# Optimization experiments

Hardware: AMD Instinct MI355X
Metric: run time of the kernel (lower is better)

The kernel has to match this reference:

```python
import jax, jax.numpy as jnp
import numpy as np

B, N, O, K, F = 4, 256, 5, 5, 256
H, D, DFF = 4, 64, 1024  # num_heads, KQ_len, FFN hidden
EPS = 1e-5


def setup_inputs() -> dict:
    key = jax.random.key(0)
    ks = jax.random.split(key, 16)
    s = 0.05
    p = lambda k, shape: (jax.random.normal(k, shape, jnp.float32) * s)
    return {
        "x": jax.random.normal(ks[0], (B, N, O, K, K, F), jnp.float32),
        "Wq": p(ks[1], (H * D, F)), "bq": p(ks[2], (H * D,)),
        "Wk": p(ks[3], (H * D, F)), "bk": p(ks[4], (H * D,)),
        "Wv": p(ks[5], (H * D, F)), "bv": p(ks[6], (H * D,)),
        "Wf": p(ks[7], (F, F)), "bf": p(ks[8], (F,)),
        "ln1_w": jnp.ones((N, O, F), jnp.float32), "ln1_b": jnp.zeros((N, O, F), jnp.float32),
        "ln2_w": jnp.ones((N, O, F), jnp.float32), "ln2_b": jnp.zeros((N, O, F), jnp.float32),
        "W1": p(ks[9], (DFF, F)), "b1": p(ks[10], (DFF,)),
        "W2": p(ks[11], (F, DFF)), "b2": p(ks[12], (F,)),
    }


def _layer_norm3(x, w, b):
    # torch LayerNorm with normalized_shape=[N, O, F]: stats over last 3 dims
    mu = jnp.mean(x, axis=(1, 2, 3), keepdims=True)
    var = jnp.var(x, axis=(1, 2, 3), keepdims=True)
    return (x - mu) * jax.lax.rsqrt(var + EPS) * w + b


def _split_heads(y):
    # [B,N,O,K,K,H*D] -> [B,N,O,H,K,K,D]
    return y.reshape(B, N, O, K, K, H, D).transpose(0, 1, 2, 5, 3, 4, 6)


def reference(x, Wq, bq, Wk, bk, Wv, bv, Wf, bf,
              ln1_w, ln1_b, ln2_w, ln2_b, W1, b1, W2, b2):
    q = _split_heads(x @ Wq.T + bq)
    k = _split_heads(x @ Wk.T + bk)
    v = _split_heads(x @ Wv.T + bv)
    c = K // 2
    qc = q[:, :, :, :, c, c, :]  # center query [B,N,O,H,D]
    # tile+mul+sum == dot of center query against every patch key
    scores = jnp.einsum('bnohd,bnohijd->bnohij', qc, k) / np.sqrt(float(D))
    w = jax.nn.softmax(scores.reshape(B, N, O, H, K * K), axis=-1)
    merged = jnp.einsum('bnohp,bnohpd->bnohd', w, v.reshape(B, N, O, H, K * K, D))
    merged = merged.reshape(B, N, O, H * D)
    attent = merged @ Wf.T + bf  # dropout = identity (eval)
    out1 = _layer_norm3(attent, ln1_w, ln1_b)
    ffn = jax.nn.relu(out1 @ W1.T + b1) @ W2.T + b2
    return _layer_norm3(out1 + ffn, ln2_w, ln2_b)
```

## Files before the change

### kernel.cpp

```cpp
#include <hip/hip_runtime.h>
#include <hip/hip_bf16.h>

#define FF 256
#define HH 4
#define DD 64
#define PP 25
#define SITES 5120
#define SPB 1280
#define DFF 1024
#define LN_ELEMS 327680

typedef const __hip_bfloat16* bfp;
typedef __hip_bfloat16* bfw;
typedef __attribute__((ext_vector_type(8))) short bf16x8;
typedef __attribute__((ext_vector_type(4))) float f32x4;

__device__ __forceinline__ float b2f(const __hip_bfloat16 v) { return __bfloat162float(v); }
__device__ __forceinline__ bool detect_bf(const unsigned* dt) {
    return dt[0] == 0x3F803F80u;
}
__device__ __forceinline__ float ldin(const void* p, size_t i, bool bf) {
    return bf ? __bfloat162float(((const __hip_bfloat16*)p)[i]) : ((const float*)p)[i];
}
__device__ __forceinline__ unsigned short f2bu(float f) {
    __hip_bfloat16 h = __float2bfloat16(f);
    return *(unsigned short*)&h;
}
__device__ __forceinline__ uint4 ldin8(const void* p, size_t i, bool bf) {
    if (bf) return *(const uint4*)((const unsigned short*)p + i);
    const float* f = (const float*)p + i;
    const float4 a = *(const float4*)f;
    const float4 b = *(const float4*)(f + 4);
    unsigned short u[8] = { f2bu(a.x), f2bu(a.y), f2bu(a.z), f2bu(a.w),
                            f2bu(b.x), f2bu(b.y), f2bu(b.z), f2bu(b.w) };
    return *(uint4*)u;
}

template<int RELU, int RES, int GATHER, int STATS, int BINT, int OUTF32>
__global__ __launch_bounds__(256) void gemm_mfma(
    const void* xg, bfp Ab, int lda,
    const void* Bm, int ldb, const void* bias,
    bfp resid, int ldr, bfw C, int ldc, int Kc,
    int aoh, size_t boh, int bioh, int coh,
    float* __restrict__ red, const unsigned* dt)
{
    const bool bf = detect_bf(dt);
    const int h = blockIdx.z;
    Ab += (size_t)h * aoh;
    const size_t boff = (size_t)h * boh;
    const size_t biasoff = (size_t)h * bioh;
    C += (size_t)h * coh;

    __shared__ unsigned short Als[64][72];
    __shared__ unsigned short Bls[64][72];
    __shared__ float rs4[4], rss4[4];
    const int tid = threadIdx.x;
    const int lane = tid & 63;
    const int w = tid >> 6;
    const int m0 = blockIdx.y * 64;
    const int n0 = blockIdx.x * 64;
    const int r8 = tid >> 3;
    const int c8 = (tid & 7) * 8;

    f32x4 acc[4];
    #pragma unroll
    for (int mi = 0; mi < 4; ++mi) acc[mi] = (f32x4){0.f, 0.f, 0.f, 0.f};

    for (int k0 = 0; k0 < Kc; k0 += 64) {
        #pragma unroll
        for (int rr = 0; rr < 2; ++rr) {
            const int row = r8 + rr * 32;
            uint4 v;
            if (GATHER) v = ldin8(xg, ((size_t)(m0 + row) * PP + 12) * FF + (k0 + c8), bf);
            else        v = *(const uint4*)(Ab + (size_t)(m0 + row) * lda + (k0 + c8));
            *(uint4*)&Als[row][c8] = v;
        }
        #pragma unroll
        for (int rr = 0; rr < 2; ++rr) {
            const int row = r8 + rr * 32;
            const size_t bi = boff + (size_t)(n0 + row) * ldb + (k0 + c8);
            uint4 v;
            if (BINT) v = *(const uint4*)((const unsigned short*)Bm + bi);
            else      v = ldin8(Bm, bi, bf);
            *(uint4*)&Bls[row][c8] = v;
        }
        __syncthreads();
        #pragma unroll
        for (int ks = 0; ks < 2; ++ks) {
            const int kq = ks * 32 + (lane >> 4) * 8;
            const bf16x8 bfr = *(const bf16x8*)&Bls[w * 16 + (lane & 15)][kq];
            #pragma unroll
            for (int mi = 0; mi < 4; ++mi) {
                const bf16x8 afr = *(const bf16x8*)&Als[mi * 16 + (lane & 15)][kq];
                acc[mi] = __builtin_amdgcn_mfma_f32_16x16x32_bf16(afr, bfr, acc[mi], 0, 0, 0);
            }
        }
        __syncthreads();
    }

    const int col = n0 + w * 16 + (lane & 15);
    const int quad = lane >> 4;
    const float bvv = (!OUTF32 && bias) ? ldin(bias, biasoff + col, bf) : 0.f;
    float s_ = 0.f, ss_ = 0.f;
    #pragma unroll
    for (int mi = 0; mi < 4; ++mi) {
        #pragma unroll
        for (int r = 0; r < 4; ++r) {
            const int row = m0 + mi * 16 + quad * 4 + r;
            float v = acc[mi][r] + bvv;
            if (OUTF32) {
                ((float*)C)[(size_t)row * ldc + col] = v;
            } else {
                if (RES)  v += b2f(resid[(size_t)row * ldr + col]);
                if (RELU) v = fmaxf(v, 0.0f);
                if (STATS) { s_ += v; ss_ += v * v; }
                C[(size_t)row * ldc + col] = __float2bfloat16(v);
            }
        }
    }
    if (STATS && !OUTF32) {
        #pragma unroll
        for (int o = 32; o > 0; o >>= 1) { s_ += __shfl_down(s_, o); ss_ += __shfl_down(ss_, o); }
        if (lane == 0) { rs4[w] = s_; rss4[w] = ss_; }
        __syncthreads();
        if (tid == 0) {
            const int batch = m0 / SPB;
            atomicAdd(&red[batch * 2 + 0], rs4[0] + rs4[1] + rs4[2] + rs4[3]);
            atomicAdd(&red[batch * 2 + 1], rss4[0] + rss4[1] + rss4[2] + rss4[3]);
        }
    }
}

__global__ __launch_bounds__(256) void prep(
    const void* Wq, const void* Wk, const void* Wv, const void* Wf,
    const void* W1, const void* W2,
    bfw WkT, bfw Wqb, bfw Wvb, bfw Wfb, bfw W1b, bfw W2b,
    const unsigned* dt)
{
    const bool bf = detect_bf(dt);
    const int idx = blockIdx.x * 256 + threadIdx.x;
    if (idx < 65536) {
        const int d = idx & 63, f = (idx >> 6) & 255, h = idx >> 14;
        WkT[idx] = __float2bfloat16(ldin(Wk, (size_t)(h * DD + d) * FF + f, bf));
    } else if (idx < 131072) {
        const int i = idx - 65536;  Wqb[i] = __float2bfloat16(ldin(Wq, i, bf));
    } else if (idx < 196608) {
        const int i = idx - 131072; Wvb[i] = __float2bfloat16(ldin(Wv, i, bf));
    } else if (idx < 262144) {
        const int i = idx - 196608; Wfb[i] = __float2bfloat16(ldin(Wf, i, bf));
    } else if (idx < 524288) {
        const int i = idx - 262144; W1b[i] = __float2bfloat16(ldin(W1, i, bf));
    } else {
        const int i = idx - 524288; W2b[i] = __float2bfloat16(ldin(W2, i, bf));
    }
}

__global__ __launch_bounds__(256) void ffn2_epi(
    const float* __restrict__ zp, bfp out1, const void* b2, bfw z,
    float* __restrict__ red, const unsigned* dt)
{
    const bool bf = detect_bf(dt);
    __shared__ float rs4[4], rss4[4];
    const int tid = threadIdx.x;
    const int i8 = (blockIdx.x * 256 + tid) * 8;
    const int col = i8 & 255;
    float v[8];
    #pragma unroll
    for (int j = 0; j < 8; ++j) v[j] = 0.f;
    #pragma unroll
    for (int kc = 0; kc < 4; ++kc) {
        const float4 a = *(const float4*)(zp + (size_t)kc * (SITES * FF) + i8);
        const float4 b = *(const float4*)(zp + (size_t)kc * (SITES * FF) + i8 + 4);
        v[0] += a.x; v[1] += a.y; v[2] += a.z; v[3] += a.w;
        v[4] += b.x; v[5] += b.y; v[6] += b.z; v[7] += b.w;
    }
    const uint4 rv = *(const uint4*)(out1 + i8);
    const unsigned short* ru = (const unsigned short*)&rv;
    float s_ = 0.f, ss_ = 0.f;
    unsigned short ou[8];
    #pragma unroll
    for (int j = 0; j < 8; ++j) {
        const float val = v[j] + ldin(b2, col + j, bf)
                        + __bfloat162float(*(const __hip_bfloat16*)&ru[j]);
        s_ += val; ss_ += val * val;
        ou[j] = f2bu(val);
    }
    *(uint4*)((unsigned short*)z + i8) = *(uint4*)ou;
    const int lane = tid & 63, w = tid >> 6;
    #pragma unroll
    for (int o = 32; o > 0; o >>= 1) { s_ += __shfl_down(s_, o); ss_ += __shfl_down(ss_, o); }
    if (lane == 0) { rs4[w] = s_; rss4[w] = ss_; }
    __syncthreads();
    if (tid == 0) {
        const int batch = (i8 >> 8) / SPB;
        atomicAdd(&red[batch * 2 + 0], rs4[0] + rs4[1] + rs4[2] + rs4[3]);
        atomicAdd(&red[batch * 2 + 1], rss4[0] + rss4[1] + rss4[2] + rss4[3]);
    }
}

__global__ __launch_bounds__(256) void attn_site(const void* x, bfp qk, bfw xw,
                                                 const unsigned* dt)
{
    __shared__ unsigned short xsb[32][264];
    __shared__ unsigned short qkb[HH][FF];
    __shared__ float sc[HH][32];
    __shared__ float wl[HH][PP];

    const bool bf = detect_bf(dt);
    const int s = blockIdx.x;
    const int t = threadIdx.x;

    const size_t xbase = (size_t)s * (PP * FF);
    for (int e0 = t * 8; e0 < PP * FF; e0 += 2048)
        *(uint4*)&xsb[e0 >> 8][e0 & 255] = ldin8(x, xbase + e0, bf);
    if (t < 128)
        ((uint4*)qkb)[t] = ((const uint4*)(qk + (size_t)s * (HH * FF)))[t];
    __syncthreads();

    if (t < 64) {
        const int lane = t;
        const int col = lane & 15;
        const int quad = lane >> 4;
        const int brow = col & 3;
        f32x4 a0v = (f32x4){0.f, 0.f, 0.f, 0.f};
        f32x4 a1v = (f32x4){0.f, 0.f, 0.f, 0.f};
        #pragma unroll
        for (int ks = 0; ks < 8; ++ks) {
            const int kq = ks * 32 + quad * 8;
            const bf16x8 bfr = *(const bf16x8*)&qkb[brow][kq];
            const bf16x8 af0 = *(const bf16x8*)&xsb[col][kq];
            const bf16x8 af1 = *(const bf16x8*)&xsb[16 + col][kq];
            a0v = __builtin_amdgcn_mfma_f32_16x16x32_bf16(af0, bfr, a0v, 0, 0, 0);
            a1v = __builtin_amdgcn_mfma_f32_16x16x32_bf16(af1, bfr, a1v, 0, 0, 0);
        }
        if (col < HH) {
            #pragma unroll
            for (int r = 0; r < 4; ++r) {
                const int p = quad * 4 + r;
                sc[col][p] = a0v[r] * 0.125f;
                const int p2 = 16 + p;
                if (p2 < PP) sc[col][p2] = a1v[r] * 0.125f;
            }
        }
    }
    __syncthreads();

    if (t < 128) {
        const int hh = t >> 5, p = t & 31;
        const float sv = (p < PP) ? sc[hh][p] : -1e30f;
        float m = sv;
        #pragma unroll
        for (int o = 16; o > 0; o >>= 1) m = fmaxf(m, __shfl_xor(m, o, 32));
        const float e = (p < PP) ? __expf(sv - m) : 0.f;
        float ssum = e;
        #pragma unroll
        for (int o = 16; o > 0; o >>= 1) ssum += __shfl_xor(ssum, o, 32);
        if (p < PP) wl[hh][p] = e / ssum;
    }
    __syncthreads();

    float a0 = 0.f, a1 = 0.f, a2 = 0.f, a3 = 0.f;
    #pragma unroll
    for (int p = 0; p < PP; ++p) {
        const float xv = __bfloat162float(*(const __hip_bfloat16*)&xsb[p][t]);
        a0 = fmaf(wl[0][p], xv, a0);
        a1 = fmaf(wl[1][p], xv, a1);
        a2 = fmaf(wl[2][p], xv, a2);
        a3 = fmaf(wl[3][p], xv, a3);
    }
    bfw xwp = xw + (size_t)s * (HH * FF) + t;
    xwp[0 * FF] = __float2bfloat16(a0);
    xwp[1 * FF] = __float2bfloat16(a1);
    xwp[2 * FF] = __float2bfloat16(a2);
    xwp[3 * FF] = __float2bfloat16(a3);
}

template<int FINAL>
__global__ __launch_bounds__(256) void ln_apply(bfp X, const float* __restrict__ red,
                                                const void* w, const void* b,
                                                void* out, const unsigned* dt)
{
    const bool bf = detect_bf(dt);
    const int i8 = (blockIdx.x * 256 + threadIdx.x) * 8;
    const int s = i8 >> 8;
    const int batch = s / SPB;
    const int r = s - batch * SPB;
    const int f = i8 & 255;
    const float inv = 1.f / (float)LN_ELEMS;
    const float mu = red[batch * 2] * inv;
    const float var = red[batch * 2 + 1] * inv - mu * mu;
    const float rs = rsqrtf(var + 1e-5f);

    const uint4 xv = *(const uint4*)(X + i8);
    const uint4 wv = ldin8(w, (size_t)r * FF + f, bf);
    const uint4 bv = ldin8(b, (size_t)r * FF + f, bf);
    const unsigned short* xu = (const unsigned short*)&xv;
    const unsigned short* wu = (const unsigned short*)&wv;
    const unsigned short* bu = (const unsigned short*)&bv;
    float vo[8];
    #pragma unroll
    for (int j = 0; j < 8; ++j) {
        const float xf = __bfloat162float(*(const __hip_bfloat16*)&xu[j]);
        const float wf = __bfloat162float(*(const __hip_bfloat16*)&wu[j]);
        const float bf2 = __bfloat162float(*(const __hip_bfloat16*)&bu[j]);
        vo[j] = (xf - mu) * rs * wf + bf2;
    }
    if (FINAL && !bf) {
        float* o = (float*)out + i8;
        *(float4*)o = (float4){vo[0], vo[1], vo[2], vo[3]};
        *(float4*)(o + 4) = (float4){vo[4], vo[5], vo[6], vo[7]};
    } else {
        unsigned short ou[8];
        #pragma unroll
        for (int j = 0; j < 8; ++j) ou[j] = f2bu(vo[j]);
        *(uint4*)((unsigned short*)out + i8) = *(uint4*)ou;
    }
}

extern "C" void kernel_launch(void* const* d_in, const int* in_sizes, int n_in,
                              void* d_out, int out_size, void* d_ws, size_t ws_size,
                              hipStream_t stream)
{
    const void* x    = d_in[0];
    const void* Wq   = d_in[1];
    const void* bq   = d_in[2];
    const void* Wk   = d_in[3];
    const void* Wv   = d_in[5];
    const void* bv   = d_in[6];
    const void* Wf   = d_in[7];
    const void* bfv  = d_in[8];
    const void* ln1w = d_in[9];
    const void* ln1b = d_in[10];
    const void* ln2w = d_in[11];
    const void* ln2b = d_in[12];
    const void* W1   = d_in[13];
    const void* b1   = d_in[14];
    const void* W2   = d_in[15];
    const void* b2   = d_in[16];
    const unsigned* dt = (const unsigned*)d_in[9];

    char* w8 = (char*)d_ws;
    bfw qk   = (bfw)(w8);
    bfw xw   = (bfw)(w8 + 10485760);
    bfw hid  = (bfw)(w8 + 20971520);
    bfw WkT  = (bfw)(w8 + 31457280);
    bfw Wqb  = (bfw)(w8 + 31588352);
    bfw Wvb  = (bfw)(w8 + 31719424);
    bfw Wfb  = (bfw)(w8 + 31850496);
    bfw W1b  = (bfw)(w8 + 31981568);
    bfw W2b  = (bfw)(w8 + 32505856);
    bfw qc   = (bfw)(w8 + 33030144);
    bfw att  = (bfw)(w8 + 35651584);
    bfw out1 = (bfw)(w8 + 38273024);
    bfw z    = (bfw)(w8 + 40894464);
    float* red = (float*)(w8 + 43515904);
    float* zp  = (float*)(w8 + 44040192);

    hipMemsetAsync(red, 0, 64, stream);

    prep<<<3072, 256, 0, stream>>>(Wq, Wk, Wv, Wf, W1, W2,
                                   WkT, Wqb, Wvb, Wfb, W1b, W2b, dt);

    gemm_mfma<0, 0, 1, 0, 1, 0><<<dim3(4, 80), 256, 0, stream>>>(
        x, nullptr, 0, Wqb, FF, bq, nullptr, 0, qc, FF, FF, 0, 0, 0, 0, nullptr, dt);

    gemm_mfma<0, 0, 0, 0, 1, 0><<<dim3(4, 80, HH), 256, 0, stream>>>(
        nullptr, qc, FF, WkT, DD, nullptr, nullptr, 0, qk, HH * FF, DD,
        DD, (size_t)FF * DD, 0, FF, nullptr, dt);

    attn_site<<<SITES, 256, 0, stream>>>(x, qk, xw, dt);

    gemm_mfma<0, 0, 0, 0, 1, 0><<<dim3(1, 80, HH), 256, 0, stream>>>(
        nullptr, xw, HH * FF, Wvb, FF, bv, nullptr, 0, qc, FF, FF,
        FF, (size_t)DD * FF, DD, DD, nullptr, dt);

    gemm_mfma<0, 0, 0, 1, 1, 0><<<dim3(4, 80), 256, 0, stream>>>(
        nullptr, qc, FF, Wfb, FF, bfv, nullptr, 0, att, FF, FF,
        0, 0, 0, 0, red, dt);

    ln_apply<0><<<640, 256, 0, stream>>>(att, red, ln1w, ln1b, out1, dt);

    gemm_mfma<1, 0, 0, 0, 1, 0><<<dim3(16, 80), 256, 0, stream>>>(
        nullptr, out1, FF, W1b, FF, b1, nullptr, 0, hid, DFF, FF,
        0, 0, 0, 0, nullptr, dt);

    gemm_mfma<0, 0, 0, 0, 1, 1><<<dim3(4, 80, 4), 256, 0, stream>>>(
        nullptr, hid, DFF, W2b, DFF, nullptr, nullptr, 0, (bfw)zp, FF, 256,
        256, 256, 0, SITES * FF * 2, nullptr, dt);

    ffn2_epi<<<640, 256, 0, stream>>>(zp, out1, b2, z, red + 8, dt);

    ln_apply<1><<<640, 256, 0, stream>>>(z, red + 8, ln2w, ln2b, d_out, dt);
}
```

Before: 328.9 us.

## Fuse query-key projection into attention kernel and drop memset launch

Removes the separate GEMM that projected the center query through Wk into a per-site qk buffer. Each attention block now computes its own 4x256 qk vector from the center query and WkT with scalar FMAs before the MFMA scoring. The reduction buffer is zeroed inside prep instead of by a separate memset. This cuts one kernel launch and a 10 MB round trip through global memory, but every one of 5120 blocks reads all 128 KB of WkT, likely from L2, and does about 64K scalar FMAs with per-element bf16 conversions.

```diff
diff --git a/kernel.cpp b/kernel.cpp
--- a/kernel.cpp
+++ b/kernel.cpp
@@ -135,9 +135,10 @@
     const void* Wq, const void* Wk, const void* Wv, const void* Wf,
     const void* W1, const void* W2,
     bfw WkT, bfw Wqb, bfw Wvb, bfw Wfb, bfw W1b, bfw W2b,
-    const unsigned* dt)
+    float* __restrict__ red, const unsigned* dt)
 {
     const bool bf = detect_bf(dt);
+    if (blockIdx.x == 0 && threadIdx.x < 16) red[threadIdx.x] = 0.f;
     const int idx = blockIdx.x * 256 + threadIdx.x;
     if (idx < 65536) {
         const int d = idx & 63, f = (idx >> 6) & 255, h = idx >> 14;
@@ -198,10 +199,11 @@
     }
 }
 
-__global__ __launch_bounds__(256) void attn_site(const void* x, bfp qk, bfw xw,
-                                                 const unsigned* dt)
+__global__ __launch_bounds__(256) void attn_site(const void* x, bfp qc, bfp WkT,
+                                                 bfw xw, const unsigned* dt)
 {
     __shared__ unsigned short xsb[32][264];
+    __shared__ unsigned short qcb[FF];
     __shared__ unsigned short qkb[HH][FF];
     __shared__ float sc[HH][32];
     __shared__ float wl[HH][PP];
@@ -213,8 +215,28 @@
     const size_t xbase = (size_t)s * (PP * FF);
     for (int e0 = t * 8; e0 < PP * FF; e0 += 2048)
         *(uint4*)&xsb[e0 >> 8][e0 & 255] = ldin8(x, xbase + e0, bf);
-    if (t < 128)
-        ((uint4*)qkb)[t] = ((const uint4*)(qk + (size_t)s * (HH * FF)))[t];
+    if (t < 32)
+        ((uint4*)qcb)[t] = ((const uint4*)(qc + (size_t)s * FF))[t];
+    __syncthreads();
+
+    #pragma unroll
+    for (int hh = 0; hh < HH; ++hh) {
+        const unsigned short* wrow = (const unsigned short*)WkT
+                                   + ((size_t)(hh * FF + t)) * DD;
+        float acc = 0.f;
+        #pragma unroll
+        for (int dc = 0; dc < 8; ++dc) {
+            const bf16x8 wv = *(const bf16x8*)(wrow + dc * 8);
+            const unsigned short* wu = (const unsigned short*)&wv;
+            #pragma unroll
+            for (int j = 0; j < 8; ++j) {
+                const float wf = __bfloat162float(*(const __hip_bfloat16*)&wu[j]);
+                const float qf = __bfloat162float(*(const __hip_bfloat16*)&qcb[hh * 64 + dc * 8 + j]);
+                acc = fmaf(wf, qf, acc);
+            }
+        }
+        qkb[hh][t] = f2bu(acc);
+    }
     __syncthreads();
 
     if (t < 64) {
@@ -340,7 +362,6 @@
     const unsigned* dt = (const unsigned*)d_in[9];
 
     char* w8 = (char*)d_ws;
-    bfw qk   = (bfw)(w8);
     bfw xw   = (bfw)(w8 + 10485760);
     bfw hid  = (bfw)(w8 + 20971520);
     bfw WkT  = (bfw)(w8 + 31457280);
@@ -356,19 +377,13 @@
     float* red = (float*)(w8 + 43515904);
     float* zp  = (float*)(w8 + 44040192);
 
-    hipMemsetAsync(red, 0, 64, stream);
-
     prep<<<3072, 256, 0, stream>>>(Wq, Wk, Wv, Wf, W1, W2,
-                                   WkT, Wqb, Wvb, Wfb, W1b, W2b, dt);
+                                   WkT, Wqb, Wvb, Wfb, W1b, W2b, red, dt);
 
     gemm_mfma<0, 0, 1, 0, 1, 0><<<dim3(4, 80), 256, 0, stream>>>(
         x, nullptr, 0, Wqb, FF, bq, nullptr, 0, qc, FF, FF, 0, 0, 0, 0, nullptr, dt);
 
-    gemm_mfma<0, 0, 0, 0, 1, 0><<<dim3(4, 80, HH), 256, 0, stream>>>(
-        nullptr, qc, FF, WkT, DD, nullptr, nullptr, 0, qk, HH * FF, DD,
-        DD, (size_t)FF * DD, 0, FF, nullptr, dt);
-
-    attn_site<<<SITES, 256, 0, stream>>>(x, qk, xw, dt);
+    attn_site<<<SITES, 256, 0, stream>>>(x, qc, WkT, xw, dt);
 
     gemm_mfma<0, 0, 0, 0, 1, 0><<<dim3(1, 80, HH), 256, 0, stream>>>(
         nullptr, xw, HH * FF, Wvb, FF, bv, nullptr, 0, qc, FF, FF,
```

Measured after the change: 413.0 us. +25.6%, slower.
